# Optimization experiments

Hardware: AMD Instinct MI355X
Metric: run time of the kernel (lower is better)

Reference implementation:

```python
import math
import jax, jax.numpy as jnp
import numpy as np

B, H, L, D = 32, 8, 4096, 64
FACTOR = 5


def setup_inputs() -> dict:
    key = jax.random.key(0)
    kq, kk, kv, ki = jax.random.split(key, 4)
    U_part = min(FACTOR * int(math.ceil(math.log(L))), L)  # 45
    return {
        "queries": jax.random.normal(kq, (B, H, L, D), jnp.float32),
        "keys": jax.random.normal(kk, (B, H, L, D), jnp.float32),
        "values": jax.random.normal(kv, (B, H, L, D), jnp.float32),
        "index_sample": jax.random.randint(ki, (L, U_part), 0, L),
        "attn_mask": jnp.ones((1,), bool),  # presence flag only
    }


def reference(queries, keys, values, index_sample, attn_mask):
    Bq, Hq, L_Q, Dd = queries.shape
    L_K = keys.shape[2]
    u = min(FACTOR * int(math.ceil(math.log(L_Q))), L_Q)
    scale = 1.0 / math.sqrt(Dd)

    # --- _prob_QK: sample K columns per query, score sparsity measure M ---
    K_sample = jnp.take(keys, index_sample, axis=2)            # [B,H,L_Q,sample_k,D]
    Q_K_sample = jnp.einsum('bhqd,bhqkd->bhqk', queries, K_sample)
    M = Q_K_sample.max(axis=-1) - Q_K_sample.mean(axis=-1)     # [B,H,L_Q]
    M_top = jnp.argsort(M, axis=-1)[:, :, -u:]                 # [B,H,u]
    Q_reduce = jnp.take_along_axis(queries, M_top[..., None], axis=2)  # [B,H,u,D]
    scores = jnp.einsum('bhqd,bhkd->bhqk', Q_reduce, keys) * scale      # [B,H,u,L_K]

    # --- ProbMask (mask_flag=True, attn_mask present): causal mask gathered at M_top ---
    causal = jnp.triu(jnp.ones((L_Q, L_K), dtype=bool), k=1)   # [L_Q,L_K]
    mask = causal[M_top]                                       # [B,H,u,L_K]
    scores = jnp.where(mask, -jnp.inf, scores)

    attn = jax.nn.softmax(scores, axis=-1)                     # [B,H,u,L_K]

    # --- initial context: cumulative sum of V (causal mean surrogate) ---
    context = jnp.cumsum(values, axis=2)                       # [B,H,L_Q,D]

    # --- scatter the attended values at the selected top-u query positions ---
    bi = jnp.arange(Bq)[:, None, None]
    hi = jnp.arange(Hq)[None, :, None]
    upd = jnp.einsum('bhqk,bhkd->bhqd', attn, values)          # [B,H,u,D]
    context = context.at[bi, hi, M_top].set(upd)

    return jnp.transpose(context, (0, 2, 1, 3))                # [B,L_Q,H,D]
```

## Files before the change

kernel.cpp:

```cpp
#include <hip/hip_runtime.h>
#include <hip/hip_bf16.h>

#define B_  32
#define H_  8
#define L_  4096
#define D_  64
#define BH_ 256
#define U_  45
#define UP_ 48

typedef float f32x4  __attribute__((ext_vector_type(4)));
typedef short bf16x8 __attribute__((ext_vector_type(8)));

__device__ __forceinline__ unsigned short f2bf(float f) {
  unsigned u = __builtin_bit_cast(unsigned, f);
  u += 0x7fffu + ((u >> 16) & 1u);
  return (unsigned short)(u >> 16);
}

__global__ __launch_bounds__(256) void k_probM(
    const float* __restrict__ Qg, const float* __restrict__ Kg,
    const int* __restrict__ idxg, float* __restrict__ Mg)
{
  const int blk   = blockIdx.x;
  const int xcd   = blk & 7;
  const int rr    = blk >> 3;
  const int bhi   = rr >> 6;
  const int chunk = rr & 63;
  const int bh    = xcd + (bhi << 3);
  const int quad  = threadIdx.x >> 2;
  const int lq    = threadIdx.x & 3;
  const int q     = chunk * 64 + quad;

  const float* qrow = Qg + ((size_t)bh * L_ + q) * D_ + lq * 16;
  double qd[16];
#pragma unroll
  for (int c = 0; c < 4; c++) {
    f32x4 v = *(const f32x4*)(qrow + 4 * c);
    qd[4*c+0] = (double)v[0]; qd[4*c+1] = (double)v[1];
    qd[4*c+2] = (double)v[2]; qd[4*c+3] = (double)v[3];
  }

  const float* kb = Kg + (size_t)bh * L_ * D_ + lq * 16;
  const int*   ip = idxg + q * U_;

  double mx = -1e300, sm = 0.0;
  for (int j = 0; j < U_; j++) {
    const float* kr = kb + (size_t)ip[j] * D_;
    double acc = 0.0;
#pragma unroll
    for (int c = 0; c < 4; c++) {
      f32x4 v = *(const f32x4*)(kr + 4 * c);
      acc += qd[4*c+0] * (double)v[0];
      acc += qd[4*c+1] * (double)v[1];
      acc += qd[4*c+2] * (double)v[2];
      acc += qd[4*c+3] * (double)v[3];
    }
    acc += __shfl_xor(acc, 1);
    acc += __shfl_xor(acc, 2);
    mx = fmax(mx, acc);
    sm += acc;
  }
  if (lq == 0) Mg[(size_t)bh * L_ + q] = (float)(mx - sm / 45.0);
}

__global__ __launch_bounds__(256) void k_top45(
    const float* __restrict__ Mg, int* __restrict__ qselg)
{
  __shared__ float mv[L_];
  __shared__ float rv[256];
  __shared__ int   ri[256];
  __shared__ int   sels[UP_];
  const int bh = blockIdx.x, t = threadIdx.x;

  for (int i = t; i < L_; i += 256) mv[i] = Mg[(size_t)bh * L_ + i];
  __syncthreads();

  for (int it = 0; it < U_; it++) {
    float bv = -3.4e38f; int bi = 0;
    for (int i = t; i < L_; i += 256) {
      float v = mv[i];
      if (v > bv) { bv = v; bi = i; }
    }
    rv[t] = bv; ri[t] = bi;
    __syncthreads();
    for (int s = 128; s > 0; s >>= 1) {
      if (t < s) {
        float ov = rv[t + s];
        if (ov > rv[t] || (ov == rv[t] && ri[t + s] < ri[t])) {
          rv[t] = ov; ri[t] = ri[t + s];
        }
      }
      __syncthreads();
    }
    if (t == 0) { sels[it] = ri[0]; mv[ri[0]] = -3.4e38f; }
    __syncthreads();
  }
  if (t == 0) { sels[45] = sels[0]; sels[46] = sels[0]; sels[47] = sels[0]; }
  __syncthreads();
  if (t < UP_) qselg[bh * UP_ + t] = sels[t];
}

__global__ __launch_bounds__(512) void k_cumsum(
    const float* __restrict__ Vg, float* __restrict__ out)
{
  const int bh = blockIdx.x, b = bh >> 3, h = bh & 7;
  const int d = threadIdx.x & 63, s = threadIdx.x >> 6;
  __shared__ float segsum[8][64];

  const float* vb = Vg + (size_t)bh * L_ * D_ + d;
  const int l0 = s * 512;

  float acc = 0.f;
  for (int l = l0; l < l0 + 512; l += 4) {
    float a0 = vb[(size_t)(l + 0) * D_];
    float a1 = vb[(size_t)(l + 1) * D_];
    float a2 = vb[(size_t)(l + 2) * D_];
    float a3 = vb[(size_t)(l + 3) * D_];
    acc += a0; acc += a1; acc += a2; acc += a3;
  }
  segsum[s][d] = acc;
  __syncthreads();

  float run = 0.f;
  for (int ss = 0; ss < s; ss++) run += segsum[ss][d];

  float* ob = out + ((size_t)b * L_ * H_ + h) * D_ + d;
  for (int l = l0; l < l0 + 512; l += 4) {
    float a0 = vb[(size_t)(l + 0) * D_];
    float a1 = vb[(size_t)(l + 1) * D_];
    float a2 = vb[(size_t)(l + 2) * D_];
    float a3 = vb[(size_t)(l + 3) * D_];
    run += a0; ob[(size_t)(l + 0) * (H_ * D_)] = run;
    run += a1; ob[(size_t)(l + 1) * (H_ * D_)] = run;
    run += a2; ob[(size_t)(l + 2) * (H_ * D_)] = run;
    run += a3; ob[(size_t)(l + 3) * (H_ * D_)] = run;
  }
}

__global__ __launch_bounds__(512, 2) void k_attn(
    const float* __restrict__ Qg, const float* __restrict__ Kg,
    const float* __restrict__ Vg, const int* __restrict__ qselg,
    float* __restrict__ out)
{
  const int bh = blockIdx.x, b = bh >> 3, h = bh & 7;
  const int wave = threadIdx.x >> 6, lane = threadIdx.x & 63;
  const int l15 = lane & 15, l4 = lane >> 4;

  __shared__ int   qs[UP_];
  __shared__ float mw[8][UP_];
  __shared__ float lw[8][UP_];
  __shared__ float lgf[UP_];
  __shared__ float Osum[UP_][64];
  __shared__ unsigned short Pl[8][16][72];

  if (threadIdx.x < UP_) qs[threadIdx.x] = qselg[bh * UP_ + threadIdx.x];
  for (int i = threadIdx.x; i < UP_ * 64; i += 512) (&Osum[0][0])[i] = 0.f;
  __syncthreads();

  int qmax = 0;
  for (int r2 = 0; r2 < UP_; r2++) qmax = max(qmax, qs[r2]);

  const float* Qb = Qg + (size_t)bh * L_ * D_;
  const float* Kb = Kg + (size_t)bh * L_ * D_;
  const float* Vb = Vg + (size_t)bh * L_ * D_;

  bf16x8 aq[3][2];
#pragma unroll
  for (int mf = 0; mf < 3; mf++) {
    const float* src = Qb + (size_t)qs[mf * 16 + l15] * D_ + l4 * 8;
#pragma unroll
    for (int ks = 0; ks < 2; ks++) {
      bf16x8 a;
#pragma unroll
      for (int j = 0; j < 8; j++) a[j] = (short)f2bf(src[ks * 32 + j]);
      aq[mf][ks] = a;
    }
  }

  int myq[3][4];
#pragma unroll
  for (int mf = 0; mf < 3; mf++)
#pragma unroll
    for (int rg = 0; rg < 4; rg++)
      myq[mf][rg] = qs[mf * 16 + l4 * 4 + rg];

  float m_r[3][4], l_r[3][4];
  f32x4 Oa[3][4];
  const f32x4 z4 = {0.f, 0.f, 0.f, 0.f};
#pragma unroll
  for (int mf = 0; mf < 3; mf++)
#pragma unroll
    for (int rg = 0; rg < 4; rg++) { m_r[mf][rg] = -1e30f; l_r[mf][rg] = 0.f; }
#pragma unroll
  for (int mf = 0; mf < 3; mf++)
#pragma unroll
    for (int df = 0; df < 4; df++) Oa[mf][df] = z4;

  for (int t = 0; t < 8; t++) {
    const int k0 = wave * 512 + t * 64;
    if (k0 > qmax) break;

    f32x4 S[3][4];
#pragma unroll
    for (int nf = 0; nf < 4; nf++) {
      const float* ksrc = Kb + (size_t)(k0 + nf * 16 + l15) * D_ + l4 * 8;
      bf16x8 bk0, bk1;
#pragma unroll
      for (int j = 0; j < 8; j++) bk0[j] = (short)f2bf(ksrc[j]);
#pragma unroll
      for (int j = 0; j < 8; j++) bk1[j] = (short)f2bf(ksrc[32 + j]);
#pragma unroll
      for (int mf = 0; mf < 3; mf++) {
        f32x4 c = z4;
        c = __builtin_amdgcn_mfma_f32_16x16x32_bf16(aq[mf][0], bk0, c, 0, 0, 0);
        c = __builtin_amdgcn_mfma_f32_16x16x32_bf16(aq[mf][1], bk1, c, 0, 0, 0);
        S[mf][nf] = c;
      }
    }

#pragma unroll
    for (int mf = 0; mf < 3; mf++)
#pragma unroll
      for (int nf = 0; nf < 4; nf++) {
        const int kc = k0 + nf * 16 + l15;
#pragma unroll
        for (int rg = 0; rg < 4; rg++) {
          float v = S[mf][nf][rg] * 0.125f;
          S[mf][nf][rg] = (kc > myq[mf][rg]) ? -1e30f : v;
        }
      }

    bf16x8 vv[2][4];
#pragma unroll
    for (int ks = 0; ks < 2; ks++)
#pragma unroll
      for (int df = 0; df < 4; df++) {
        bf16x8 x;
#pragma unroll
        for (int j = 0; j < 8; j++)
          x[j] = (short)f2bf(Vb[(size_t)(k0 + ks * 32 + l4 * 8 + j) * D_ + df * 16 + l15]);
        vv[ks][df] = x;
      }

#pragma unroll
    for (int mf = 0; mf < 3; mf++) {
#pragma unroll
      for (int rg = 0; rg < 4; rg++) {
        float tm = fmax(fmax(S[mf][0][rg], S[mf][1][rg]),
                        fmax(S[mf][2][rg], S[mf][3][rg]));
#pragma unroll
        for (int off = 1; off < 16; off <<= 1) tm = fmax(tm, __shfl_xor(tm, off));
        const float mn = fmax(m_r[mf][rg], tm);
        const float sc = __expf(m_r[mf][rg] - mn);
        l_r[mf][rg] *= sc;
#pragma unroll
        for (int df = 0; df < 4; df++) Oa[mf][df][rg] *= sc;
        m_r[mf][rg] = mn;
      }

      float rs[4] = {0.f, 0.f, 0.f, 0.f};
#pragma unroll
      for (int nf = 0; nf < 4; nf++)
#pragma unroll
        for (int rg = 0; rg < 4; rg++) {
          float p = __expf(S[mf][nf][rg] - m_r[mf][rg]);
          p = (m_r[mf][rg] > -1e29f) ? p : 0.f;
          rs[rg] += p;
          Pl[wave][l4 * 4 + rg][nf * 16 + l15] = f2bf(p);
        }
#pragma unroll
      for (int rg = 0; rg < 4; rg++) {
        float r = rs[rg];
#pragma unroll
        for (int off = 1; off < 16; off <<= 1) r += __shfl_xor(r, off);
        l_r[mf][rg] += r;
      }

#pragma unroll
      for (int ks = 0; ks < 2; ks++) {
        const bf16x8 pa = *(const bf16x8*)(&Pl[wave][l15][ks * 32 + l4 * 8]);
#pragma unroll
        for (int df = 0; df < 4; df++)
          Oa[mf][df] = __builtin_amdgcn_mfma_f32_16x16x32_bf16(pa, vv[ks][df], Oa[mf][df], 0, 0, 0);
      }
    }
  }

  if (l15 == 0) {
#pragma unroll
    for (int mf = 0; mf < 3; mf++)
#pragma unroll
      for (int rg = 0; rg < 4; rg++) {
        const int row = mf * 16 + l4 * 4 + rg;
        mw[wave][row] = m_r[mf][rg];
        lw[wave][row] = l_r[mf][rg];
      }
  }
  __syncthreads();

  float sc_me[3][4];
#pragma unroll
  for (int mf = 0; mf < 3; mf++)
#pragma unroll
    for (int rg = 0; rg < 4; rg++) {
      const int row = mf * 16 + l4 * 4 + rg;
      float m = -1e30f;
#pragma unroll
      for (int w = 0; w < 8; w++) m = fmax(m, mw[w][row]);
      float ls = 0.f;
#pragma unroll
      for (int w = 0; w < 8; w++) ls += lw[w][row] * __expf(mw[w][row] - m);
      sc_me[mf][rg] = __expf(m_r[mf][rg] - m);
      if (wave == 0 && l15 == 0) lgf[row] = ls;
    }

  for (int w = 0; w < 8; w++) {
    __syncthreads();
    if (wave == w) {
#pragma unroll
      for (int mf = 0; mf < 3; mf++)
#pragma unroll
        for (int df = 0; df < 4; df++)
#pragma unroll
          for (int rg = 0; rg < 4; rg++)
            Osum[mf * 16 + l4 * 4 + rg][df * 16 + l15] += Oa[mf][df][rg] * sc_me[mf][rg];
    }
  }
  __syncthreads();

  for (int i = threadIdx.x; i < U_ * 64; i += 512) {
    const int r = i >> 6, d = i & 63;
    out[(((size_t)b * L_ + (size_t)qs[r]) * H_ + h) * D_ + d] = Osum[r][d] / lgf[r];
  }
}

extern "C" void kernel_launch(void* const* d_in, const int* in_sizes, int n_in,
                              void* d_out, int out_size, void* d_ws, size_t ws_size,
                              hipStream_t stream)
{
  const float* Q   = (const float*)d_in[0];
  const float* K   = (const float*)d_in[1];
  const float* V   = (const float*)d_in[2];
  const int*   idx = (const int*)d_in[3];
  float* out = (float*)d_out;

  const size_t m_bytes = (size_t)BH_ * L_ * sizeof(float);
  float* M    = (float*)d_ws;
  int*   qsel = (int*)((char*)d_ws + m_bytes);
  if (ws_size < m_bytes + (size_t)BH_ * UP_ * sizeof(int)) return;

  k_probM <<<16384, 256, 0, stream>>>(Q, K, idx, M);
  k_top45 <<<BH_,   256, 0, stream>>>(M, qsel);
  k_cumsum<<<BH_,   512, 0, stream>>>(V, out);
  k_attn  <<<BH_,   512, 0, stream>>>(Q, K, V, qsel, out);
}
```

Measured before the change: 1.286 ms.

## Rewrite probM kernel with fp32 math, 8-lane dot products and prefetched gathers

```diff
diff --git a/kernel.cpp b/kernel.cpp
--- a/kernel.cpp
+++ b/kernel.cpp
@@ -18,50 +18,85 @@
   return (unsigned short)(u >> 16);
 }
 
-__global__ __launch_bounds__(256) void k_probM(
+__global__ __launch_bounds__(256, 4) void k_probM(
     const float* __restrict__ Qg, const float* __restrict__ Kg,
     const int* __restrict__ idxg, float* __restrict__ Mg)
 {
   const int blk   = blockIdx.x;
   const int xcd   = blk & 7;
   const int rr    = blk >> 3;
-  const int bhi   = rr >> 6;
-  const int chunk = rr & 63;
+  const int bhi   = rr >> 7;
+  const int chunk = rr & 127;
   const int bh    = xcd + (bhi << 3);
-  const int quad  = threadIdx.x >> 2;
-  const int lq    = threadIdx.x & 3;
-  const int q     = chunk * 64 + quad;
-
-  const float* qrow = Qg + ((size_t)bh * L_ + q) * D_ + lq * 16;
-  double qd[16];
-#pragma unroll
-  for (int c = 0; c < 4; c++) {
-    f32x4 v = *(const f32x4*)(qrow + 4 * c);
-    qd[4*c+0] = (double)v[0]; qd[4*c+1] = (double)v[1];
-    qd[4*c+2] = (double)v[2]; qd[4*c+3] = (double)v[3];
-  }
-
-  const float* kb = Kg + (size_t)bh * L_ * D_ + lq * 16;
-  const int*   ip = idxg + q * U_;
-
-  double mx = -1e300, sm = 0.0;
-  for (int j = 0; j < U_; j++) {
-    const float* kr = kb + (size_t)ip[j] * D_;
-    double acc = 0.0;
-#pragma unroll
-    for (int c = 0; c < 4; c++) {
-      f32x4 v = *(const f32x4*)(kr + 4 * c);
-      acc += qd[4*c+0] * (double)v[0];
-      acc += qd[4*c+1] * (double)v[1];
-      acc += qd[4*c+2] * (double)v[2];
-      acc += qd[4*c+3] * (double)v[3];
-    }
-    acc += __shfl_xor(acc, 1);
-    acc += __shfl_xor(acc, 2);
-    mx = fmax(mx, acc);
-    sm += acc;
-  }
-  if (lq == 0) Mg[(size_t)bh * L_ + q] = (float)(mx - sm / 45.0);
+  const int q0    = chunk * 32;
+
+  __shared__ int sidx[32 * U_];
+  for (int i = threadIdx.x; i < 32 * U_; i += 256)
+    sidx[i] = idxg[(size_t)q0 * U_ + i];
+  __syncthreads();
+
+  const int qq = threadIdx.x >> 3;
+  const int o  = threadIdx.x & 7;
+  const int q  = q0 + qq;
+
+  const float* qrow = Qg + ((size_t)bh * L_ + q) * D_ + o * 8;
+  const f32x4 qa = *(const f32x4*)qrow;
+  const f32x4 qb = *(const f32x4*)(qrow + 4);
+
+  const float* kb = Kg + (size_t)bh * L_ * D_ + o * 8;
+  const int* myidx = &sidx[qq * U_];
+
+#define FETCHIDS(ID, G) \
+  _Pragma("unroll") \
+  for (int r = 0; r < 5; r++) ID[r] = myidx[(G) * 5 + r];
+
+#define LOADG(R0, R1, IDS) \
+  _Pragma("unroll") \
+  for (int r = 0; r < 5; r++) { \
+    const float* kr = kb + (size_t)IDS[r] * D_; \
+    R0[r] = *(const f32x4*)kr; \
+    R1[r] = *(const f32x4*)(kr + 4); \
+  }
+
+#define COMPUTE(R0, R1) \
+  _Pragma("unroll") \
+  for (int r = 0; r < 5; r++) { \
+    float e0 = fmaf(qa[0], R0[r][0], fmaf(qa[1], R0[r][1], \
+               fmaf(qa[2], R0[r][2], qa[3] * R0[r][3]))); \
+    float e1 = fmaf(qb[0], R1[r][0], fmaf(qb[1], R1[r][1], \
+               fmaf(qb[2], R1[r][2], qb[3] * R1[r][3]))); \
+    float d = e0 + e1; \
+    d += __shfl_xor(d, 1); \
+    d += __shfl_xor(d, 2); \
+    d += __shfl_xor(d, 4); \
+    mx = fmax(mx, d); sm += d; \
+  }
+
+  int ida[5], idb[5];
+  FETCHIDS(ida, 0);
+  FETCHIDS(idb, 1);
+
+  f32x4 A0[5], A1[5], B0[5], B1[5];
+  LOADG(A0, A1, ida);
+  FETCHIDS(ida, 2);
+
+  float mx = -3.4e38f, sm = 0.f;
+#pragma unroll
+  for (int gp = 0; gp < 4; gp++) {
+    LOADG(B0, B1, idb);
+    COMPUTE(A0, A1);
+    if (gp < 3) { FETCHIDS(idb, 2 * gp + 3); }
+    LOADG(A0, A1, ida);
+    COMPUTE(B0, B1);
+    if (gp < 3) { FETCHIDS(ida, 2 * gp + 4); }
+  }
+  COMPUTE(A0, A1);
+
+#undef FETCHIDS
+#undef LOADG
+#undef COMPUTE
+
+  if (o == 0) Mg[(size_t)bh * L_ + q] = mx - sm * (1.0f / 45.0f);
 }
 
 __global__ __launch_bounds__(256) void k_top45(
@@ -350,7 +385,7 @@
   int*   qsel = (int*)((char*)d_ws + m_bytes);
   if (ws_size < m_bytes + (size_t)BH_ * UP_ * sizeof(int)) return;
 
-  k_probM <<<16384, 256, 0, stream>>>(Q, K, idx, M);
+  k_probM <<<32768, 256, 0, stream>>>(Q, K, idx, M);
   k_top45 <<<BH_,   256, 0, stream>>>(M, qsel);
   k_cumsum<<<BH_,   512, 0, stream>>>(V, out);
   k_attn  <<<BH_,   512, 0, stream>>>(Q, K, V, qsel, out);
```

Result: slower. 1.521 ms (+18.3%).

## Rewrite probM as wave-per-query-group with double-buffered LDS gather and fp32

Applied to the files above, without the earlier changes.

```diff
diff --git a/kernel.cpp b/kernel.cpp
--- a/kernel.cpp
+++ b/kernel.cpp
@@ -18,50 +18,116 @@
   return (unsigned short)(u >> 16);
 }
 
-__global__ __launch_bounds__(256) void k_probM(
+#define WAITV(N) asm volatile("s_waitcnt vmcnt(" #N ")" ::: "memory")
+#define SCHEDB() __builtin_amdgcn_sched_barrier(0)
+
+__global__ __launch_bounds__(64) void k_probM(
     const float* __restrict__ Qg, const float* __restrict__ Kg,
     const int* __restrict__ idxg, float* __restrict__ Mg)
 {
   const int blk   = blockIdx.x;
   const int xcd   = blk & 7;
   const int rr    = blk >> 3;
-  const int bhi   = rr >> 6;
-  const int chunk = rr & 63;
+  const int bhi   = rr >> 9;
+  const int chunk = rr & 511;
   const int bh    = xcd + (bhi << 3);
-  const int quad  = threadIdx.x >> 2;
-  const int lq    = threadIdx.x & 3;
-  const int q     = chunk * 64 + quad;
-
-  const float* qrow = Qg + ((size_t)bh * L_ + q) * D_ + lq * 16;
-  double qd[16];
-#pragma unroll
-  for (int c = 0; c < 4; c++) {
-    f32x4 v = *(const f32x4*)(qrow + 4 * c);
-    qd[4*c+0] = (double)v[0]; qd[4*c+1] = (double)v[1];
-    qd[4*c+2] = (double)v[2]; qd[4*c+3] = (double)v[3];
-  }
-
-  const float* kb = Kg + (size_t)bh * L_ * D_ + lq * 16;
-  const int*   ip = idxg + q * U_;
-
-  double mx = -1e300, sm = 0.0;
-  for (int j = 0; j < U_; j++) {
-    const float* kr = kb + (size_t)ip[j] * D_;
-    double acc = 0.0;
-#pragma unroll
-    for (int c = 0; c < 4; c++) {
-      f32x4 v = *(const f32x4*)(kr + 4 * c);
-      acc += qd[4*c+0] * (double)v[0];
-      acc += qd[4*c+1] * (double)v[1];
-      acc += qd[4*c+2] * (double)v[2];
-      acc += qd[4*c+3] * (double)v[3];
-    }
-    acc += __shfl_xor(acc, 1);
-    acc += __shfl_xor(acc, 2);
-    mx = fmax(mx, acc);
-    sm += acc;
-  }
-  if (lq == 0) Mg[(size_t)bh * L_ + q] = (float)(mx - sm / 45.0);
+  const int q0    = chunk * 8;
+
+  const int lane = threadIdx.x;
+  const int sig  = lane & 15;
+  const int rgrp = lane >> 4;
+  const int jrow = (lane < U_) ? lane : (U_ - 1);
+  const int jx   = jrow & 7;
+  const int idxlane = (lane < U_) ? lane : (U_ - 1);
+
+  __shared__ float kbuf0[48 * 64];
+  __shared__ float kbuf1[48 * 64];
+  __shared__ float qbuf[64];
+
+  const float* Kb = Kg + (size_t)bh * (L_ * D_);
+  const float* Qb = Qg + (size_t)bh * (L_ * D_);
+
+#define PREF(IDXV, QV, QABS) do { \
+    (IDXV) = idxg[(size_t)(QABS) * U_ + idxlane]; \
+    (QV)   = *(const f32x4*)(Qb + (size_t)(QABS) * D_ + (sig << 2)); \
+  } while (0)
+
+#define STAGE(BUF, IDXV) do { \
+    _Pragma("unroll") \
+    for (int g = 0; g < 12; g++) { \
+      const int r_  = 4 * g + rgrp; \
+      const int rc_ = (r_ < U_) ? r_ : (U_ - 1); \
+      const int kid = __shfl((IDXV), rc_); \
+      const int c_  = sig ^ (r_ & 7); \
+      const float* gp_ = Kb + (size_t)kid * D_ + (c_ << 2); \
+      __builtin_amdgcn_global_load_lds( \
+          (const __attribute__((address_space(1))) void*)gp_, \
+          (__attribute__((address_space(3))) void*)((BUF) + g * 256), \
+          16, 0, 0); \
+    } \
+  } while (0)
+
+#define COMPUTE(BUF, QV, QI) do { \
+    if (lane < 16) *(f32x4*)(qbuf + (sig << 2)) = (QV); \
+    float dacc = 0.f; \
+    _Pragma("unroll") \
+    for (int g = 0; g < 16; g++) { \
+      f32x4 kv = *(const f32x4*)((BUF) + jrow * 64 + ((g ^ jx) << 2)); \
+      f32x4 qq = *(const f32x4*)(qbuf + (g << 2)); \
+      dacc = fmaf(kv[0], qq[0], dacc); \
+      dacc = fmaf(kv[1], qq[1], dacc); \
+      dacc = fmaf(kv[2], qq[2], dacc); \
+      dacc = fmaf(kv[3], qq[3], dacc); \
+    } \
+    float mxv = (lane < U_) ? dacc : -3.4e38f; \
+    float smv = (lane < U_) ? dacc : 0.f; \
+    _Pragma("unroll") \
+    for (int off = 1; off < 64; off <<= 1) { \
+      mxv = fmax(mxv, __shfl_xor(mxv, off)); \
+      smv += __shfl_xor(smv, off); \
+    } \
+    if (lane == 0) Mg[(size_t)bh * L_ + q0 + (QI)] = mxv - smv * (1.0f / 45.0f); \
+  } while (0)
+
+  int   idxT; f32x4 qvT;
+  PREF(idxT, qvT, q0 + 0);
+  WAITV(0);
+  SCHEDB();
+  f32x4 qvC = qvT;
+  int   idxS = idxT;
+  int   idxN; f32x4 qvN;
+  PREF(idxN, qvN, q0 + 1);
+  SCHEDB();
+  STAGE(kbuf0, idxS);
+  SCHEDB();
+
+#pragma unroll
+  for (int qi = 0; qi < 8; qi++) {
+    float* bufC = (qi & 1) ? kbuf1 : kbuf0;
+    float* bufS = (qi & 1) ? kbuf0 : kbuf1;
+
+    if (qi == 0)      { WAITV(12); }
+    else if (qi < 7)  { WAITV(13); }
+    SCHEDB();
+    int   idxStage = idxN;
+    f32x4 qvNext   = qvN;
+
+    if (qi < 6) { PREF(idxN, qvN, q0 + qi + 2); SCHEDB(); }
+    if (qi < 7) { STAGE(bufS, idxStage); SCHEDB(); }
+
+    if (qi < 6)       { WAITV(14); }
+    else if (qi == 6) { WAITV(12); }
+    else              { WAITV(0);  }
+    SCHEDB();
+
+    COMPUTE(bufC, qvC, qi);
+    SCHEDB();
+    qvC = qvNext;
+  }
+
+#undef PREF
+#undef STAGE
+#undef COMPUTE
 }
 
 __global__ __launch_bounds__(256) void k_top45(
@@ -350,8 +416,8 @@
   int*   qsel = (int*)((char*)d_ws + m_bytes);
   if (ws_size < m_bytes + (size_t)BH_ * UP_ * sizeof(int)) return;
 
-  k_probM <<<16384, 256, 0, stream>>>(Q, K, idx, M);
-  k_top45 <<<BH_,   256, 0, stream>>>(M, qsel);
-  k_cumsum<<<BH_,   512, 0, stream>>>(V, out);
-  k_attn  <<<BH_,   512, 0, stream>>>(Q, K, V, qsel, out);
-}
+  k_probM <<<131072, 64, 0, stream>>>(Q, K, idx, M);
+  k_top45 <<<BH_,    256, 0, stream>>>(M, qsel);
+  k_cumsum<<<BH_,    512, 0, stream>>>(V, out);
+  k_attn  <<<BH_,    512, 0, stream>>>(Q, K, V, qsel, out);
+}
```

Result: slower. 1.673 ms (+30.1%).

## Software-pipeline sampled K gathers in probM with fp32 math and LDS indices

Applied to the files above, without the earlier changes.

```diff
diff --git a/kernel.cpp b/kernel.cpp
--- a/kernel.cpp
+++ b/kernel.cpp
@@ -18,7 +18,7 @@
   return (unsigned short)(u >> 16);
 }
 
-__global__ __launch_bounds__(256) void k_probM(
+__global__ __launch_bounds__(256, 3) void k_probM(
     const float* __restrict__ Qg, const float* __restrict__ Kg,
     const int* __restrict__ idxg, float* __restrict__ Mg)
 {
@@ -28,40 +28,77 @@
   const int bhi   = rr >> 6;
   const int chunk = rr & 63;
   const int bh    = xcd + (bhi << 3);
+  const int q0    = chunk * 64;
   const int quad  = threadIdx.x >> 2;
   const int lq    = threadIdx.x & 3;
-  const int q     = chunk * 64 + quad;
+  const int q     = q0 + quad;
+
+  __shared__ int sidx[U_][65];
+  for (int i = threadIdx.x; i < 64 * U_; i += 256) {
+    const int qq = i / U_, j = i - qq * U_;
+    sidx[j][qq] = idxg[(size_t)q0 * U_ + i];
+  }
+  __syncthreads();
 
   const float* qrow = Qg + ((size_t)bh * L_ + q) * D_ + lq * 16;
-  double qd[16];
-#pragma unroll
-  for (int c = 0; c < 4; c++) {
-    f32x4 v = *(const f32x4*)(qrow + 4 * c);
-    qd[4*c+0] = (double)v[0]; qd[4*c+1] = (double)v[1];
-    qd[4*c+2] = (double)v[2]; qd[4*c+3] = (double)v[3];
-  }
-
-  const float* kb = Kg + (size_t)bh * L_ * D_ + lq * 16;
-  const int*   ip = idxg + q * U_;
-
-  double mx = -1e300, sm = 0.0;
-  for (int j = 0; j < U_; j++) {
-    const float* kr = kb + (size_t)ip[j] * D_;
-    double acc = 0.0;
-#pragma unroll
-    for (int c = 0; c < 4; c++) {
-      f32x4 v = *(const f32x4*)(kr + 4 * c);
-      acc += qd[4*c+0] * (double)v[0];
-      acc += qd[4*c+1] * (double)v[1];
-      acc += qd[4*c+2] * (double)v[2];
-      acc += qd[4*c+3] * (double)v[3];
-    }
-    acc += __shfl_xor(acc, 1);
-    acc += __shfl_xor(acc, 2);
-    mx = fmax(mx, acc);
-    sm += acc;
-  }
-  if (lq == 0) Mg[(size_t)bh * L_ + q] = (float)(mx - sm / 45.0);
+  f32x4 qv[4];
+#pragma unroll
+  for (int c = 0; c < 4; c++) qv[c] = *(const f32x4*)(qrow + 4 * c);
+
+  const float* kb = Kg + (size_t)bh * (L_ * D_) + lq * 16;
+
+#define LOADROW(R, ID) do { \
+    const float* kr_ = kb + ((size_t)(ID) << 6); \
+    R[0] = *(const f32x4*)(kr_);      R[1] = *(const f32x4*)(kr_ + 4); \
+    R[2] = *(const f32x4*)(kr_ + 8);  R[3] = *(const f32x4*)(kr_ + 12); \
+  } while (0)
+
+#define DOTROW(R) do { \
+    float e0_ = 0.f, e1_ = 0.f; \
+    _Pragma("unroll") \
+    for (int c_ = 0; c_ < 4; c_++) { \
+      e0_ = fmaf(qv[c_][0], R[c_][0], e0_); \
+      e1_ = fmaf(qv[c_][1], R[c_][1], e1_); \
+      e0_ = fmaf(qv[c_][2], R[c_][2], e0_); \
+      e1_ = fmaf(qv[c_][3], R[c_][3], e1_); \
+    } \
+    float d_ = e0_ + e1_; \
+    d_ += __shfl_xor(d_, 1); \
+    d_ += __shfl_xor(d_, 2); \
+    mx = fmax(mx, d_); sm += d_; \
+  } while (0)
+
+  int idA0 = sidx[0][quad], idA1 = sidx[1][quad];
+  int idB0 = sidx[2][quad], idB1 = sidx[3][quad];
+
+  f32x4 A0[4], A1[4], B0[4], B1[4];
+  LOADROW(A0, idA0);
+  LOADROW(A1, idA1);
+
+  float mx = -3.4e38f, sm = 0.f;
+#pragma unroll 1
+  for (int t = 0; t < 11; t++) {
+    LOADROW(B0, idB0);
+    LOADROW(B1, idB1);
+    const int ga = 4 * t + 4, gb = 4 * t + 5;
+    const int nA0 = sidx[ga < U_ ? ga : U_ - 1][quad];
+    const int nA1 = sidx[gb < U_ ? gb : U_ - 1][quad];
+    DOTROW(A0);
+    DOTROW(A1);
+    LOADROW(A0, nA0);
+    LOADROW(A1, nA1);
+    const int gc = 4 * t + 6, gd = 4 * t + 7;
+    idB0 = sidx[gc < U_ ? gc : U_ - 1][quad];
+    idB1 = sidx[gd < U_ ? gd : U_ - 1][quad];
+    DOTROW(B0);
+    DOTROW(B1);
+  }
+  DOTROW(A0);
+
+#undef LOADROW
+#undef DOTROW
+
+  if (lq == 0) Mg[(size_t)bh * L_ + q] = mx - sm * (1.0f / 45.0f);
 }
 
 __global__ __launch_bounds__(256) void k_top45(
```

Result: slower. 1.500 ms (+16.6%).
